# Optimization experiments

Measured on AMD Instinct MI355X. Metric: run time of the kernel, lower is better.

## Reference

```python
import jax, jax.numpy as jnp
import numpy as np

RADIUS = 2.0      # ball radius (meters)
NSAMPLE = 32      # max neighbors per ball
B = 4             # number of scenes (batch)
NPB = 4096        # points per scene (equal counts assumed)
C = 20            # number of semantic classes
CUBE = 20.0       # points live in a [0,20]^3 m cube


def setup_inputs() -> dict:
    key = jax.random.key(0)
    k1, k2, k3 = jax.random.split(key, 3)
    xyz = jax.random.uniform(k1, (B * NPB, 3), jnp.float32) * CUBE
    pred = jax.random.normal(k2, (B * NPB, C), jnp.float32)
    labels = jax.random.randint(k3, (B * NPB,), 0, C)
    tgt = jax.nn.one_hot(labels, C, dtype=jnp.float32)
    cnt = jnp.full((B,), NPB, dtype=jnp.int32)
    # module asserts new_xyz == xyz and equal batch counts
    return {"xyz": xyz, "xyz_batch_cnt": cnt, "pred": pred, "tgt": tgt,
            "new_xyz": xyz, "new_xyz_batch_cnt": cnt}


def _ball_query(xyz_b, new_xyz_b, radius, nsample):
    """xyz_b, new_xyz_b: (B, n, 3). Returns local idx (B, n, nsample).
    Replicates pointnet2 stack ball_query: first `nsample` points (in index
    order) with squared distance < radius^2; unfilled slots repeat the first
    found index. Indices are local to each batch segment."""
    n = xyz_b.shape[1]
    d2 = jnp.sum((new_xyz_b[:, :, None, :] - xyz_b[:, None, :, :]) ** 2, axis=-1)  # (B,n,n)
    mask = d2 < radius * radius
    # score = point index if inside ball else sentinel n; smallest scores = first hits
    score = jnp.where(mask, jnp.arange(n, dtype=jnp.int32), jnp.int32(n))
    neg_vals, _ = jax.lax.top_k(-score, nsample)   # largest of -score == smallest score
    idx = -neg_vals                                # (B,n,nsample), ascending index order
    first = idx[:, :, :1]                          # first found index (self is always in-ball)
    idx = jnp.where(idx == n, first, idx)          # fill empty slots with first index
    return idx


def _group(feats_b, idx_b):
    """feats_b: (B, n, C); idx_b: (B, m, nsample) local indices -> (B, m, nsample, C)."""
    b = jnp.arange(feats_b.shape[0])[:, None, None]
    return feats_b[b, idx_b]


def reference(xyz, xyz_batch_cnt, pred, tgt, new_xyz, new_xyz_batch_cnt):
    nb = xyz_batch_cnt.shape[0]
    n = xyz.shape[0] // nb                 # equal per-batch counts
    xyz_b = xyz.reshape(nb, n, 3)
    new_xyz_b = new_xyz.reshape(nb, n, 3)

    idx_b = _ball_query(xyz_b, new_xyz_b, RADIUS, NSAMPLE)   # (B,n,ns)
    m = nb * n
    idx = idx_b.reshape(m, NSAMPLE)

    # grouping_operation -> (M, C, nsample)
    grouped_pred = _group(pred.reshape(nb, n, -1), idx_b).reshape(m, NSAMPLE, -1).transpose(0, 2, 1)
    grouped_tgt = _group(tgt.reshape(nb, n, -1), idx_b).reshape(m, NSAMPLE, -1).transpose(0, 2, 1)

    # since new_xyz == xyz, every ball contains its own center -> empty_ball_mask
    # is all-False and the nonempty filtering in the torch code is the identity.
    pred_local_relation = grouped_pred - pred[:, :, None]
    tgt_local_relation = grouped_tgt - tgt[:, :, None]

    # weight (computed under no_grad in torch)
    eq = idx == idx[:, :1]
    not_eq = ~eq
    not_eq = not_eq.at[:, 0].set(True)
    a = not_eq.astype(jnp.float32)
    weight = a / jnp.sum(a, axis=-1, keepdims=True)
    return (pred_local_relation, tgt_local_relation, weight)
```

## Files before the change

### kernel.cpp

```cpp
#include <hip/hip_runtime.h>

#define NS 32
#define GD 10
#define NCXY (GD * GD)
#define COLCAP 128
#define WCAP 64
#define INV_CELL 0.5f
#define MARGIN 1e-3f

static __device__ __forceinline__ int lane_rank(unsigned long long m) {
    return __builtin_amdgcn_mbcnt_hi((unsigned)(m >> 32),
                                     __builtin_amdgcn_mbcnt_lo((unsigned)m, 0u));
}

__global__ __launch_bounds__(256) void build_kernel(
    const float* __restrict__ xyz, int n,
    int* __restrict__ colOff, float4* __restrict__ pts)
{
    __shared__ float4 hl[4][WCAP];
    __shared__ int    swcnt[4];
    __shared__ float4 merged[COLCAP];

    const int col  = blockIdx.x;
    const int b    = col / NCXY;
    const int cxy  = col - b * NCXY;
    const int mycx = cxy / GD;
    const int mycy = cxy - mycx * GD;
    const int lane = threadIdx.x & 63;
    const int wv   = threadIdx.x >> 6;
    const float* __restrict__ px = xyz + (size_t)b * n * 3;

    const int per = (n + 3) >> 2;
    const int j0  = wv * per;
    const int j1  = min(j0 + per, n);
    int cnt = 0;
    for (int it = j0; it < j1; it += 64) {
        const int  j   = it + lane;
        const bool inb = j < j1;
        const int  jc  = inb ? j : 0;
        const float x = px[3 * jc], y = px[3 * jc + 1], z = px[3 * jc + 2];
        const int cx = min(max((int)floorf(x * INV_CELL), 0), GD - 1);
        const int cy = min(max((int)floorf(y * INV_CELL), 0), GD - 1);
        const bool hit = inb && (cx == mycx) && (cy == mycy);
        const unsigned long long m = __ballot(hit);
        if (m) {
            const int zc  = min(max((int)floorf(z * INV_CELL), 0), GD - 1);
            const int pos = cnt + lane_rank(m);
            if (hit && pos < WCAP)
                hl[wv][pos] = make_float4(x, y, z, __int_as_float((zc << 12) | j));
            cnt += __popcll(m);
        }
    }
    if (lane == 0) swcnt[wv] = cnt < WCAP ? cnt : WCAP;
    __syncthreads();

    const int p0 = swcnt[0], p1 = p0 + swcnt[1], p2 = p1 + swcnt[2], p3 = p2 + swcnt[3];
    const int h  = p3 < COLCAP ? p3 : COLCAP;
    if (wv == 0) {
        for (int g = lane; g < h; g += 64) {
            const int w   = (g >= p0) + (g >= p1) + (g >= p2);
            const int off = g - (w == 0 ? 0 : (w == 1 ? p0 : (w == 2 ? p1 : p2)));
            merged[g] = hl[w][off];
        }
    }
    __syncthreads();

    if (wv == 0) {
        int czc[GD];
        #pragma unroll
        for (int k = 0; k < GD; ++k) czc[k] = 0;
        for (int r = 0; r < h; r += 64) {
            const int t = r + lane;
            int zc = -1;
            if (t < h) zc = __float_as_int(merged[t].w) >> 12;
            #pragma unroll
            for (int k = 0; k < GD; ++k)
                czc[k] += __popcll(__ballot(zc == k));
        }
        int off[GD + 1];
        off[0] = 0;
        #pragma unroll
        for (int k = 0; k < GD; ++k) off[k + 1] = off[k] + czc[k];

        int cur[GD];
        #pragma unroll
        for (int k = 0; k < GD; ++k) cur[k] = off[k];

        for (int r = 0; r < h; r += 64) {
            const int t = r + lane;
            int zc = -1, pl = 0;
            float4 f = make_float4(0.f, 0.f, 0.f, 0.f);
            if (t < h) { f = merged[t]; pl = __float_as_int(f.w); zc = pl >> 12; }
            #pragma unroll
            for (int k = 0; k < GD; ++k) {
                const unsigned long long mk = __ballot(zc == k);
                if (zc == k) {
                    const int pos = cur[k] + lane_rank(mk);
                    pts[(size_t)col * COLCAP + pos] =
                        make_float4(f.x, f.y, f.z, __int_as_float(pl & 4095));
                }
                cur[k] += __popcll(mk);
            }
        }
        if (lane == 0) {
            const int bo = col * 11;
            #pragma unroll
            for (int k = 0; k < GD; ++k) colOff[bo + k] = off[k];
            colOff[bo + GD] = h;
        }
    }
}

template <int C>
__global__ __launch_bounds__(256) void query_kernel(
    const float* __restrict__ new_xyz,
    const float* __restrict__ pred, const float* __restrict__ tgt,
    const int* __restrict__ colOff, const float4* __restrict__ pts,
    int n, int total,
    float* __restrict__ out0, float* __restrict__ out1, float* __restrict__ wout)
{
#pragma clang fp contract(off)
    __shared__ int slist[4][64];
    __shared__ int sorted[4][64];

    const int lane = threadIdx.x & 63;
    const int wv   = __builtin_amdgcn_readfirstlane(threadIdx.x >> 6);
    int q = blockIdx.x * 4 + wv;
    if (q >= total) q = total - 1;
    const int b    = q / n;
    const int base = b * n;

    const float qx = new_xyz[q * 3 + 0];
    const float qy = new_xyz[q * 3 + 1];
    const float qz = new_xyz[q * 3 + 2];

    int cx0 = max((int)floorf((qx - 2.0f - MARGIN) * INV_CELL), 0);
    int cx1 = min((int)floorf((qx + 2.0f + MARGIN) * INV_CELL), GD - 1);
    int cy0 = max((int)floorf((qy - 2.0f - MARGIN) * INV_CELL), 0);
    int cy1 = min((int)floorf((qy + 2.0f + MARGIN) * INV_CELL), GD - 1);
    int cz0 = max((int)floorf((qz - 2.0f - MARGIN) * INV_CELL), 0);
    int cz1 = min((int)floorf((qz + 2.0f + MARGIN) * INV_CELL), GD - 1);
    const int ny = cy1 - cy0 + 1;
    const int nrange = __builtin_amdgcn_readfirstlane((cx1 - cx0 + 1) * ny);

    int cc = 0, gb = 0;
    if (lane < nrange) {
        const int rx   = lane / ny;
        const int ry   = lane - rx * ny;
        const int ccol = b * NCXY + (cx0 + rx) * GD + (cy0 + ry);
        const int o0   = colOff[ccol * 11 + cz0];
        const int o1   = colOff[ccol * 11 + cz1 + 1];
        gb = ccol * COLCAP + o0;
        cc = o1 - o0;
    }
    int run = cc;
    #pragma unroll
    for (int off = 1; off < 64; off <<= 1) {
        int y = __shfl_up(run, off, 64);
        if (lane >= off) run += y;
    }
    const int T = __shfl(run, nrange - 1, 64);

    int tot = 0;
    for (int r = 0; r < T; r += 128) {
        const int  tA   = r + lane;
        const int  tB   = tA + 64;
        const bool actA = tA < T;
        const bool actB = tB < T;
        const int  tca  = actA ? tA : 0;
        const int  tcb  = actB ? tB : 0;
        int kA = 0, kB = 0;
        #pragma unroll
        for (int step = 8; step >= 1; step >>= 1) {
            const int pA = __shfl(run, kA + step - 1, 64);
            const int pB = __shfl(run, kB + step - 1, 64);
            if (pA <= tca) kA += step;
            if (pB <= tcb) kB += step;
        }
        const int pmA = __shfl(run, (kA > 0 ? kA : 1) - 1, 64);
        const int pmB = __shfl(run, (kB > 0 ? kB : 1) - 1, 64);
        const int prefA = kA > 0 ? pmA : 0;
        const int prefB = kB > 0 ? pmB : 0;
        const int gbA = __shfl(gb, kA, 64);
        const int gbB = __shfl(gb, kB, 64);
        const float4 fA = pts[gbA + (tca - prefA)];
        const float4 fB = pts[gbB + (tcb - prefB)];

        float dxA = qx - fA.x, dyA = qy - fA.y, dzA = qz - fA.z;
        const float d2A = (dxA * dxA + dyA * dyA) + dzA * dzA;
        float dxB = qx - fB.x, dyB = qy - fB.y, dzB = qz - fB.z;
        const float d2B = (dxB * dxB + dyB * dyB) + dzB * dzB;
        const bool hitA = actA && (d2A < 4.0f);
        const bool hitB = actB && (d2B < 4.0f);

        const unsigned long long mA = __ballot(hitA);
        const int posA = tot + lane_rank(mA);
        if (hitA && posA < 64) slist[wv][posA] = __float_as_int(fA.w);
        tot += __popcll(mA);
        const unsigned long long mB = __ballot(hitB);
        const int posB = tot + lane_rank(mB);
        if (hitB && posB < 64) slist[wv][posB] = __float_as_int(fB.w);
        tot += __popcll(mB);
    }

    __syncthreads();

    const int totv = tot < 64 ? tot : 64;
    int v = (lane < totv) ? slist[wv][lane] : 0x7fffffff;

    if (totv <= 32) {
        int rank = 0;
        #pragma unroll
        for (int k = 0; k < 32; ++k) {
            const int vk = __shfl(v, k, 64);
            rank += ((vk < v) || (vk == v && k < lane)) ? 1 : 0;
        }
        if (lane < 32) sorted[wv][rank] = v;
    } else {
        #pragma unroll
        for (int k = 2; k <= 64; k <<= 1) {
            #pragma unroll
            for (int j = k >> 1; j >= 1; j >>= 1) {
                const int  o     = __shfl_xor(v, j, 64);
                const bool up    = ((lane & k) == 0);
                const bool lower = ((lane & j) == 0);
                const int  mn = v < o ? v : o;
                const int  mx = v < o ? o : v;
                v = (lower == up) ? mn : mx;
            }
        }
        sorted[wv][lane] = v;
    }

    __syncthreads();

    const int tc    = tot < NS ? tot : NS;
    const int s     = lane & 31;
    const int jl0   = sorted[wv][s];
    const int first = (tot > 0) ? sorted[wv][0] : (n - 1);
    const int jl    = (s < tc) ? jl0 : first;

    const int tcm = tc > 0 ? tc : 1;
    if (lane < NS)
        wout[(size_t)q * NS + lane] = (lane < tcm) ? 1.0f / (float)tcm : 0.0f;

    const float* __restrict__ src = (lane >> 5) ? tgt : pred;
    float* __restrict__ dst       = (lane >> 5) ? out1 : out0;
    const float4* __restrict__ nb = (const float4*)(src + (size_t)(base + jl) * C);
    const float4* __restrict__ ct = (const float4*)(src + (size_t)q * C);
    float* __restrict__ o = dst + (size_t)q * (C * NS) + s;
    #pragma unroll
    for (int c4 = 0; c4 < C / 4; ++c4) {
        const float4 a = nb[c4], bq = ct[c4];
        o[(c4 * 4 + 0) * NS] = a.x - bq.x;
        o[(c4 * 4 + 1) * NS] = a.y - bq.y;
        o[(c4 * 4 + 2) * NS] = a.z - bq.z;
        o[(c4 * 4 + 3) * NS] = a.w - bq.w;
    }
    #pragma unroll
    for (int c = (C / 4) * 4; c < C; ++c)
        o[c * NS] = src[(size_t)(base + jl) * C + c] - src[(size_t)q * C + c];
}

template <int C>
__global__ __launch_bounds__(256) void fused_brute_kernel(
    const float* __restrict__ xyz, const float* __restrict__ new_xyz,
    const float* __restrict__ pred, const float* __restrict__ tgt,
    int n, int total, float* __restrict__ out0, float* __restrict__ out1,
    float* __restrict__ wout)
{
#pragma clang fp contract(off)
    __shared__ int sidx[8][NS];

    const int lane = threadIdx.x & 63;
    const int wv   = __builtin_amdgcn_readfirstlane(threadIdx.x >> 6);
    int q0 = (blockIdx.x * 4 + wv) * 2;
    if (q0 > total - 2) q0 = total - 2;
    const int base = (q0 / n) * n;

    const float ax0 = new_xyz[q0 * 3 + 0], ay0 = new_xyz[q0 * 3 + 1], az0 = new_xyz[q0 * 3 + 2];
    const float ax1 = new_xyz[q0 * 3 + 3], ay1 = new_xyz[q0 * 3 + 4], az1 = new_xyz[q0 * 3 + 5];
    const float* __restrict__ px = xyz + (size_t)base * 3;

    int tot0 = 0, tot1 = 0, first0 = n - 1, first1 = n - 1;
    for (int it = 0; it < n; it += 64) {
        const int ja  = it + lane;
        const int jca = ja < n ? ja : n - 1;
        const float xa = px[jca * 3 + 0], ya = px[jca * 3 + 1], za = px[jca * 3 + 2];
        float dx = ax0 - xa, dy = ay0 - ya, dz = az0 - za;
        const float d0 = (dx * dx + dy * dy) + dz * dz;
        dx = ax1 - xa; dy = ay1 - ya; dz = az1 - za;
        const float d1 = (dx * dx + dy * dy) + dz * dz;
        const bool h0 = (ja < n) & (d0 < 4.0f);
        const bool h1 = (ja < n) & (d1 < 4.0f);
        const unsigned long long m0 = __ballot(h0);
        if (m0) {
            if (tot0 == 0) first0 = it + __builtin_ctzll(m0);
            const int pos = tot0 + lane_rank(m0);
            if (h0 && pos < NS) sidx[wv * 2 + 0][pos] = ja;
            tot0 += __popcll(m0);
        }
        const unsigned long long m1 = __ballot(h1);
        if (m1) {
            if (tot1 == 0) first1 = it + __builtin_ctzll(m1);
            const int pos = tot1 + lane_rank(m1);
            if (h1 && pos < NS) sidx[wv * 2 + 1][pos] = ja;
            tot1 += __popcll(m1);
        }
    }

    const int s  = lane & 31;
    const int qs = lane >> 5;
    {
        const int tt    = qs ? tot1 : tot0;
        const int first = qs ? first1 : first0;
        const int tc    = tt < NS ? tt : NS;
        if (s >= tc) sidx[wv * 2 + qs][s] = first;
        const int tcm = tc > 0 ? tc : 1;
        wout[(size_t)q0 * NS + lane] = (s < tcm) ? 1.0f / (float)tcm : 0.0f;
    }
    __syncthreads();

    const int q  = q0 + qs;
    const int jl = sidx[wv * 2 + qs][s];
    const float4* __restrict__ nb_p = (const float4*)(pred + (size_t)(base + jl) * C);
    const float4* __restrict__ nb_t = (const float4*)(tgt  + (size_t)(base + jl) * C);
    const float4* __restrict__ ct_p = (const float4*)(pred + (size_t)q * C);
    const float4* __restrict__ ct_t = (const float4*)(tgt  + (size_t)q * C);
    float* __restrict__ o0 = out0 + (size_t)q * (C * NS) + s;
    float* __restrict__ o1 = out1 + (size_t)q * (C * NS) + s;
    #pragma unroll
    for (int c4 = 0; c4 < C / 4; ++c4) {
        const float4 a = nb_p[c4], bq = ct_p[c4];
        o0[(c4 * 4 + 0) * NS] = a.x - bq.x;
        o0[(c4 * 4 + 1) * NS] = a.y - bq.y;
        o0[(c4 * 4 + 2) * NS] = a.z - bq.z;
        o0[(c4 * 4 + 3) * NS] = a.w - bq.w;
        const float4 u = nb_t[c4], vv = ct_t[c4];
        o1[(c4 * 4 + 0) * NS] = u.x - vv.x;
        o1[(c4 * 4 + 1) * NS] = u.y - vv.y;
        o1[(c4 * 4 + 2) * NS] = u.z - vv.z;
        o1[(c4 * 4 + 3) * NS] = u.w - vv.w;
    }
}

extern "C" void kernel_launch(void* const* d_in, const int* in_sizes, int n_in,
                              void* d_out, int out_size, void* d_ws, size_t ws_size,
                              hipStream_t stream)
{
    const float* xyz     = (const float*)d_in[0];
    const float* pred    = (const float*)d_in[2];
    const float* tgt     = (const float*)d_in[3];
    const float* new_xyz = (const float*)d_in[4];

    const int total = in_sizes[0] / 3;
    const int nb    = in_sizes[1];
    const int n     = total / nb;
    const int C     = in_sizes[2] / total;

    float* out = (float*)d_out;
    const size_t relsz = (size_t)total * C * NS;
    float* out0 = out;
    float* out1 = out + relsz;
    float* wout = out + 2 * relsz;

    const int ncols = nb * NCXY;
    const size_t ws_need = (size_t)ncols * COLCAP * sizeof(float4)
                         + (size_t)ncols * 11 * sizeof(int);

    if (C == 20 && ws_size >= ws_need) {
        float4* pts    = (float4*)d_ws;
        int*    colOff = (int*)((char*)d_ws + (size_t)ncols * COLCAP * sizeof(float4));

        build_kernel<<<ncols, 256, 0, stream>>>(xyz, n, colOff, pts);
        query_kernel<20><<<(total + 3) / 4, 256, 0, stream>>>(
            new_xyz, pred, tgt, colOff, pts, n, total, out0, out1, wout);
    } else if (C == 20) {
        fused_brute_kernel<20><<<(total + 7) / 8, 256, 0, stream>>>(
            xyz, new_xyz, pred, tgt, n, total, out0, out1, wout);
    }
    (void)n_in; (void)out_size;
}
```

Baseline: 38.00 us.

## Split ball query and gather into separate index and group kernels

Splits the fused query kernel in two. One kernel now writes only the neighbor indices (and weights) into a workspace buffer. A new elementwise group kernel then gathers pred/tgt and writes the relation outputs with coalesced float4 stores, instead of the previous strided per-lane stores. When the workspace is too small, the index buffer is aliased onto the weight output and weights are recomputed by a separate kernel, which adds extra launches and an index round-trip through memory.

Result: slower. 49.71 us (+30.8%).

```diff
diff --git a/kernel.cpp b/kernel.cpp
--- a/kernel.cpp
+++ b/kernel.cpp
@@ -111,13 +111,11 @@
     }
 }
 
-template <int C>
-__global__ __launch_bounds__(256) void query_kernel(
+template <bool WRITE_W>
+__global__ __launch_bounds__(256) void bq_idx_kernel(
     const float* __restrict__ new_xyz,
-    const float* __restrict__ pred, const float* __restrict__ tgt,
     const int* __restrict__ colOff, const float4* __restrict__ pts,
-    int n, int total,
-    float* __restrict__ out0, float* __restrict__ out1, float* __restrict__ wout)
+    int n, int total, int* __restrict__ idxb, float* __restrict__ wout)
 {
 #pragma clang fp contract(off)
     __shared__ int slist[4][64];
@@ -234,32 +232,64 @@
 
     __syncthreads();
 
-    const int tc    = tot < NS ? tot : NS;
-    const int s     = lane & 31;
-    const int jl0   = sorted[wv][s];
-    const int first = (tot > 0) ? sorted[wv][0] : (n - 1);
-    const int jl    = (s < tc) ? jl0 : first;
-
-    const int tcm = tc > 0 ? tc : 1;
-    if (lane < NS)
-        wout[(size_t)q * NS + lane] = (lane < tcm) ? 1.0f / (float)tcm : 0.0f;
-
-    const float* __restrict__ src = (lane >> 5) ? tgt : pred;
-    float* __restrict__ dst       = (lane >> 5) ? out1 : out0;
-    const float4* __restrict__ nb = (const float4*)(src + (size_t)(base + jl) * C);
-    const float4* __restrict__ ct = (const float4*)(src + (size_t)q * C);
-    float* __restrict__ o = dst + (size_t)q * (C * NS) + s;
+    if (lane < NS) {
+        const int tc    = tot < NS ? tot : NS;
+        const int jl0   = sorted[wv][lane];
+        const int first = (tot > 0) ? sorted[wv][0] : (n - 1);
+        const int jl    = (lane < tc) ? jl0 : first;
+        idxb[(size_t)q * NS + lane] = base + jl;
+        if (WRITE_W) {
+            const int tcm = tc > 0 ? tc : 1;
+            wout[(size_t)q * NS + lane] = (lane < tcm) ? 1.0f / (float)tcm : 0.0f;
+        }
+    }
+}
+
+template <int C>
+__global__ __launch_bounds__(256) void group_kernel(
+    const float* __restrict__ pred, const float* __restrict__ tgt,
+    const int* __restrict__ idxb,
+    float* __restrict__ out0, float* __restrict__ out1, int nelem4)
+{
+    int e = blockIdx.x * 256 + threadIdx.x;
+    if (e >= nelem4) return;
+    int q   = e / (C * (NS / 4));
+    int rem = e - q * (C * (NS / 4));
+    int c   = rem >> 3;
+    int g   = rem & 7;
+
+    int4 gi = *reinterpret_cast<const int4*>(idxb + (size_t)q * NS + g * 4);
+    float pc = pred[(size_t)q * C + c];
+    float tc = tgt[(size_t)q * C + c];
+
+    float4 p, t;
+    p.x = pred[(size_t)gi.x * C + c] - pc;
+    p.y = pred[(size_t)gi.y * C + c] - pc;
+    p.z = pred[(size_t)gi.z * C + c] - pc;
+    p.w = pred[(size_t)gi.w * C + c] - pc;
+    t.x = tgt[(size_t)gi.x * C + c] - tc;
+    t.y = tgt[(size_t)gi.y * C + c] - tc;
+    t.z = tgt[(size_t)gi.z * C + c] - tc;
+    t.w = tgt[(size_t)gi.w * C + c] - tc;
+
+    reinterpret_cast<float4*>(out0)[e] = p;
+    reinterpret_cast<float4*>(out1)[e] = t;
+}
+
+__global__ __launch_bounds__(256) void weight_kernel(float* __restrict__ w, int nelem)
+{
+    int e = blockIdx.x * 256 + threadIdx.x;
+    if (e >= nelem) return;
+    int lane = threadIdx.x & 63;
+    int s    = e & 31;
+    int idx  = reinterpret_cast<int*>(w)[e];
+    int idx0 = __shfl(idx, lane & 32, 64);
+    float a = (s == 0 || idx != idx0) ? 1.0f : 0.0f;
+    float sum = a;
     #pragma unroll
-    for (int c4 = 0; c4 < C / 4; ++c4) {
-        const float4 a = nb[c4], bq = ct[c4];
-        o[(c4 * 4 + 0) * NS] = a.x - bq.x;
-        o[(c4 * 4 + 1) * NS] = a.y - bq.y;
-        o[(c4 * 4 + 2) * NS] = a.z - bq.z;
-        o[(c4 * 4 + 3) * NS] = a.w - bq.w;
-    }
-    #pragma unroll
-    for (int c = (C / 4) * 4; c < C; ++c)
-        o[c * NS] = src[(size_t)(base + jl) * C + c] - src[(size_t)q * C + c];
+    for (int off = 1; off < 32; off <<= 1)
+        sum += __shfl_xor(sum, off, 64);
+    w[e] = a / sum;
 }
 
 template <int C>
@@ -365,16 +395,31 @@
     float* wout = out + 2 * relsz;
 
     const int ncols = nb * NCXY;
-    const size_t ws_need = (size_t)ncols * COLCAP * sizeof(float4)
-                         + (size_t)ncols * 11 * sizeof(int);
-
-    if (C == 20 && ws_size >= ws_need) {
+    const size_t grid_bytes = (size_t)ncols * COLCAP * sizeof(float4)
+                            + (size_t)ncols * 11 * sizeof(int);
+    const size_t idx_bytes  = (size_t)total * NS * sizeof(int);
+    const int nelem4  = total * C * (NS / 4);
+    const int gblocks = (nelem4 + 255) / 256;
+
+    if (C == 20 && ws_size >= grid_bytes + idx_bytes) {
         float4* pts    = (float4*)d_ws;
         int*    colOff = (int*)((char*)d_ws + (size_t)ncols * COLCAP * sizeof(float4));
+        int*    idxb   = (int*)((char*)d_ws + grid_bytes);
 
         build_kernel<<<ncols, 256, 0, stream>>>(xyz, n, colOff, pts);
-        query_kernel<20><<<(total + 3) / 4, 256, 0, stream>>>(
-            new_xyz, pred, tgt, colOff, pts, n, total, out0, out1, wout);
+        bq_idx_kernel<true><<<(total + 3) / 4, 256, 0, stream>>>(
+            new_xyz, colOff, pts, n, total, idxb, wout);
+        group_kernel<20><<<gblocks, 256, 0, stream>>>(pred, tgt, idxb, out0, out1, nelem4);
+    } else if (C == 20 && ws_size >= grid_bytes) {
+        float4* pts    = (float4*)d_ws;
+        int*    colOff = (int*)((char*)d_ws + (size_t)ncols * COLCAP * sizeof(float4));
+        int*    idxb   = (int*)wout;
+
+        build_kernel<<<ncols, 256, 0, stream>>>(xyz, n, colOff, pts);
+        bq_idx_kernel<false><<<(total + 3) / 4, 256, 0, stream>>>(
+            new_xyz, colOff, pts, n, total, idxb, wout);
+        group_kernel<20><<<gblocks, 256, 0, stream>>>(pred, tgt, idxb, out0, out1, nelem4);
+        weight_kernel<<<(total * NS + 255) / 256, 256, 0, stream>>>(wout, total * NS);
     } else if (C == 20) {
         fused_brute_kernel<20><<<(total + 7) / 8, 256, 0, stream>>>(
             xyz, new_xyz, pred, tgt, n, total, out0, out1, wout);
```
